# Performance work log

Measured on AMD Instinct MI355X. Metric: run time of the kernel, lower is better.

The kernel has to match this reference:

```python
import jax, jax.numpy as jnp
import numpy as np

B, S, D = 4, 8192, 512


def log_g(x):
    # torch: where(x>=0, log(relu(x)+0.5), -softplus(-x)); relu(x)+0.5 >= 0.5 so log is safe
    return jnp.where(x >= 0, jnp.log(jax.nn.relu(x) + 0.5), -jax.nn.softplus(-x))


def parallel_scan_log(log_coeffs, log_values):
    # log_coeffs: (B,S,D); log_values: (B,S+1,D)
    a_star = jnp.pad(jnp.cumsum(log_coeffs, axis=1), ((0, 0), (1, 0), (0, 0)))  # (B,S+1,D)
    log_h = a_star + jax.lax.cumlogsumexp(log_values - a_star, axis=1)
    return jnp.exp(log_h)[:, 1:]  # (B,S,D)


def setup_inputs() -> dict:
    key = jax.random.key(0)
    ks = jax.random.split(key, 7)
    scale = 1.0 / np.sqrt(D)
    x = jax.random.normal(ks[0], (B, S, D), dtype=jnp.float32)
    pre_h = jnp.zeros((B, 1, D), dtype=jnp.float32)
    Wf = jax.random.normal(ks[1], (D, D), dtype=jnp.float32) * scale
    bf = jax.random.normal(ks[2], (D,), dtype=jnp.float32) * 0.01
    Wi = jax.random.normal(ks[3], (D, D), dtype=jnp.float32) * scale
    bi = jax.random.normal(ks[4], (D,), dtype=jnp.float32) * 0.01
    Wh = jax.random.normal(ks[5], (D, D), dtype=jnp.float32) * scale
    bh = jax.random.normal(ks[6], (D,), dtype=jnp.float32) * 0.01
    return {"x": x, "pre_h": pre_h, "Wf": Wf, "bf": bf, "Wi": Wi, "bi": bi, "Wh": Wh, "bh": bh}


def reference(x, pre_h, Wf, bf, Wi, bi, Wh, bh):
    # gates: log(sigmoid(k)) = -softplus(-k)
    log_f = -jax.nn.softplus(-(jnp.einsum('bsd,de->bse', x, Wf) + bf))
    log_i = -jax.nn.softplus(-(jnp.einsum('bsd,de->bse', x, Wi) + bi))
    log_tilde_h = log_g(jnp.einsum('bsd,de->bse', x, Wh) + bh)
    log_pre_h = log_g(pre_h)  # (B,1,D)
    log_values = jnp.concatenate([log_pre_h, log_i + log_tilde_h], axis=1)  # (B,S+1,D)
    return parallel_scan_log(log_f, log_values)
```

## Files before the change

### kernel.cpp

```cpp
#include <hip/hip_runtime.h>
#include <hip/hip_bf16.h>

#define BATCH 4
#define SEQ   8192
#define DIM   512
#define M_TOT (BATCH*SEQ)
#define NCHUNK 128
#define CLEN   64

typedef __attribute__((ext_vector_type(4))) int int4v;

__device__ __forceinline__ float sigmoidf_(float x) {
    return 1.0f / (1.0f + __expf(-x));
}
__device__ __forceinline__ float gfun_(float x) {
    return (x >= 0.0f) ? (x + 0.5f) : sigmoidf_(x);
}

__device__ __forceinline__ void stage16(const void* g, void* lds) {
    __builtin_amdgcn_global_load_lds((const __attribute__((address_space(1))) void*)g,
                                     (__attribute__((address_space(3))) void*)lds,
                                     16, 0, 0);
}

__global__ __launch_bounds__(256) void quant_x(const float* __restrict__ x,
                                               char* __restrict__ xh, char* __restrict__ xl)
{
    const int t = blockIdx.x * 256 + threadIdx.x;
    float4 v = ((const float4*)x)[t];
    float vals[4] = {v.x, v.y, v.z, v.w};
    char hs[4], ls[4];
    #pragma unroll
    for (int e = 0; e < 4; ++e) {
        float c = fminf(fmaxf(vals[e], -15.8f), 15.8f);
        int q = (int)rintf(c * 2048.0f);
        int hi = (q + 128) >> 8;
        int lo = q - (hi << 8);
        hs[e] = (char)hi; ls[e] = (char)lo;
    }
    char4 hv = {hs[0], hs[1], hs[2], hs[3]};
    char4 lv = {ls[0], ls[1], ls[2], ls[3]};
    *(char4*)&xh[(size_t)t * 4] = hv;
    *(char4*)&xl[(size_t)t * 4] = lv;
}

__global__ __launch_bounds__(256) void quant_wT(
    const float* __restrict__ Wf, const float* __restrict__ Wi, const float* __restrict__ Wh,
    char* __restrict__ wth, char* __restrict__ wtl)
{
    __shared__ float tile[64][65];
    const int g = blockIdx.z;
    const float* W = (g == 0) ? Wf : (g == 1) ? Wi : Wh;
    const int k0 = blockIdx.x * 64, n0 = blockIdx.y * 64;
    const int c = threadIdx.x & 63, r4 = threadIdx.x >> 6;
    #pragma unroll
    for (int p = 0; p < 16; ++p) {
        int r = p * 4 + r4;
        tile[r][c] = W[(size_t)(k0 + r) * DIM + n0 + c];
    }
    __syncthreads();
    const size_t gbase = (size_t)g * DIM * DIM;
    #pragma unroll
    for (int p = 0; p < 16; ++p) {
        int nr = p * 4 + r4;
        float w = tile[c][nr];
        float cl = fminf(fmaxf(w, -0.49f), 0.49f);
        int q = (int)rintf(cl * 65536.0f);
        int hi = (q + 128) >> 8;
        int lo = q - (hi << 8);
        size_t o = gbase + (size_t)(n0 + nr) * DIM + k0 + c;
        wth[o] = (char)hi;
        wtl[o] = (char)lo;
    }
}

__device__ __forceinline__ void stage_tiles(
    const char* __restrict__ xhp, const char* __restrict__ xlp,
    const char* __restrict__ whp, const char* __restrict__ wlp,
    int m0, int n0, int k0,
    char (*A)[128][64], char (*B)[128][64], int wave, int lane)
{
    #pragma unroll
    for (int it = 0; it < 2; ++it) {
        const int grp = it * 4 + wave;
        const int mm  = grp * 16 + (lane >> 2);
        const int kb  = (lane & 3) * 16;
        const int ksw = kb ^ (((mm >> 1) & 3) << 4);
        stage16(xhp + (size_t)(m0 + mm) * DIM + k0 + ksw, &A[0][grp * 16][0]);
        stage16(xlp + (size_t)(m0 + mm) * DIM + k0 + ksw, &A[1][grp * 16][0]);
        stage16(whp + (size_t)(n0 + mm) * DIM + k0 + ksw, &B[0][grp * 16][0]);
        stage16(wlp + (size_t)(n0 + mm) * DIM + k0 + ksw, &B[1][grp * 16][0]);
    }
}

__global__ __launch_bounds__(256, 2) void gemm_i8(
    const char* __restrict__ xh, const char* __restrict__ xl,
    const char* __restrict__ wth, const char* __restrict__ wtl,
    const float* __restrict__ bfv, const float* __restrict__ biv, const float* __restrict__ bhv,
    float* __restrict__ fb, unsigned short* __restrict__ sib, unsigned short* __restrict__ ghb)
{
    __shared__ char sA[2][2][128][64];
    __shared__ char sB[2][2][128][64];

    const int bid = blockIdx.x;
    const int xr  = bid & 7;
    const int t   = bid >> 3;
    const int mmt = t / 12;
    const int gn  = t - mmt * 12;
    const int g   = gn >> 2;
    const int n0  = (gn & 3) * 128;
    const int m0  = (xr + (mmt << 3)) * 128;

    const int tid  = threadIdx.x;
    const int wave = tid >> 6;
    const int lane = tid & 63;
    const int wi = wave >> 1, wj = wave & 1;

    const char* wh_g = wth + (size_t)g * DIM * DIM;
    const char* wl_g = wtl + (size_t)g * DIM * DIM;

    int4v P2[4][4], P1[4][4];
    const int4v zero = {0, 0, 0, 0};
    #pragma unroll
    for (int i = 0; i < 4; ++i)
        #pragma unroll
        for (int j = 0; j < 4; ++j) { P2[i][j] = zero; P1[i][j] = zero; }

    stage_tiles(xh, xl, wh_g, wl_g, m0, n0, 0, sA[0], sB[0], wave, lane);
    __syncthreads();

    for (int kt = 0; kt < 8; ++kt) {
        const int cur = kt & 1;
        if (kt < 7) {
            stage_tiles(xh, xl, wh_g, wl_g, m0, n0, (kt + 1) * 64,
                        sA[cur ^ 1], sB[cur ^ 1], wave, lane);
        }
        const int kseg = (lane >> 4) * 16;
        int4v bhf[4], blf[4];
        #pragma unroll
        for (int j = 0; j < 4; ++j) {
            const int col = wj * 64 + j * 16 + (lane & 15);
            const int ks  = kseg ^ (((col >> 1) & 3) << 4);
            bhf[j] = *(const int4v*)&sB[cur][0][col][ks];
            blf[j] = *(const int4v*)&sB[cur][1][col][ks];
        }
        #pragma unroll
        for (int i = 0; i < 4; ++i) {
            const int row = wi * 64 + i * 16 + (lane & 15);
            const int ks  = kseg ^ (((row >> 1) & 3) << 4);
            int4v ahf = *(const int4v*)&sA[cur][0][row][ks];
            int4v alf = *(const int4v*)&sA[cur][1][row][ks];
            #pragma unroll
            for (int j = 0; j < 4; ++j) {
                P2[i][j] = __builtin_amdgcn_mfma_i32_16x16x64_i8(ahf, bhf[j], P2[i][j], 0, 0, 0);
                P1[i][j] = __builtin_amdgcn_mfma_i32_16x16x64_i8(ahf, blf[j], P1[i][j], 0, 0, 0);
                P1[i][j] = __builtin_amdgcn_mfma_i32_16x16x64_i8(alf, bhf[j], P1[i][j], 0, 0, 0);
            }
        }
        __syncthreads();
    }

    const float c2 = 1.0f / 2048.0f;
    const float c1 = 1.0f / 524288.0f;
    const float* bias = (g == 0) ? bfv : (g == 1) ? biv : bhv;
    #pragma unroll
    for (int j = 0; j < 4; ++j) {
        const int col = n0 + wj * 64 + j * 16 + (lane & 15);
        const float bv = bias[col];
        #pragma unroll
        for (int i = 0; i < 4; ++i) {
            #pragma unroll
            for (int r = 0; r < 4; ++r) {
                const float kv = (float)P2[i][j][r] * c2 + (float)P1[i][j][r] * c1 + bv;
                const int row = m0 + wi * 64 + i * 16 + (lane >> 4) * 4 + r;
                const size_t o = (size_t)row * DIM + col;
                if (g == 0) {
                    fb[o] = sigmoidf_(kv);
                } else if (g == 1) {
                    sib[o] = (unsigned short)fminf(rintf(sigmoidf_(kv) * 65536.0f), 65535.0f);
                } else {
                    ghb[o] = (unsigned short)fminf(rintf(gfun_(kv) * 8192.0f), 65535.0f);
                }
            }
        }
    }
}

#define VSCALE (1.0f / 536870912.0f)

__global__ __launch_bounds__(256) void scan_pass1(
    const float* __restrict__ fb,
    const unsigned short* __restrict__ sib, const unsigned short* __restrict__ ghb,
    float* __restrict__ Ach, float* __restrict__ Bch)
{
    const int d = blockIdx.x * 256 + threadIdx.x;
    const int c = blockIdx.y;
    const int b = blockIdx.z;
    float A = 1.0f, Bacc = 0.0f;
    size_t base = ((size_t)(b * SEQ + c * CLEN)) * DIM + d;
    #pragma unroll 4
    for (int t = 0; t < CLEN; ++t) {
        float f = fb[base + (size_t)t * DIM];
        float v = (float)sib[base + (size_t)t * DIM] *
                  (float)ghb[base + (size_t)t * DIM] * VSCALE;
        Bacc = fmaf(f, Bacc, v);
        A *= f;
    }
    const int idx = (b * NCHUNK + c) * DIM + d;
    Ach[idx] = A;
    Bch[idx] = Bacc;
}

__global__ __launch_bounds__(256) void scan_pass2(
    const float* __restrict__ pre_h,
    const float* __restrict__ Ach, const float* __restrict__ Bch,
    float* __restrict__ carry)
{
    const int gidx = blockIdx.x * 256 + threadIdx.x;
    const int b = gidx >> 9;
    const int d = gidx & (DIM - 1);
    float h = gfun_(pre_h[b * DIM + d]);
    for (int c = 0; c < NCHUNK; ++c) {
        const int idx = (b * NCHUNK + c) * DIM + d;
        carry[idx] = h;
        h = fmaf(Ach[idx], h, Bch[idx]);
    }
}

__global__ __launch_bounds__(256) void scan_pass3(
    const float* __restrict__ fb,
    const unsigned short* __restrict__ sib, const unsigned short* __restrict__ ghb,
    const float* __restrict__ carry, float* __restrict__ out)
{
    const int d = blockIdx.x * 256 + threadIdx.x;
    const int c = blockIdx.y;
    const int b = blockIdx.z;
    float h = carry[(b * NCHUNK + c) * DIM + d];
    size_t base = ((size_t)(b * SEQ + c * CLEN)) * DIM + d;
    #pragma unroll 4
    for (int t = 0; t < CLEN; ++t) {
        float f = fb[base + (size_t)t * DIM];
        float v = (float)sib[base + (size_t)t * DIM] *
                  (float)ghb[base + (size_t)t * DIM] * VSCALE;
        h = fmaf(f, h, v);
        out[base + (size_t)t * DIM] = h;
    }
}

extern "C" void kernel_launch(void* const* d_in, const int* in_sizes, int n_in,
                              void* d_out, int out_size, void* d_ws, size_t ws_size,
                              hipStream_t stream) {
    const float* x     = (const float*)d_in[0];
    const float* pre_h = (const float*)d_in[1];
    const float* Wf    = (const float*)d_in[2];
    const float* bf    = (const float*)d_in[3];
    const float* Wi    = (const float*)d_in[4];
    const float* bi    = (const float*)d_in[5];
    const float* Wh    = (const float*)d_in[6];
    const float* bh    = (const float*)d_in[7];
    float* out = (float*)d_out;

    char* ws = (char*)d_ws;
    const size_t XQ = (size_t)M_TOT * DIM;
    const size_t WQ = (size_t)3 * DIM * DIM;
    const size_t FB = (size_t)M_TOT * DIM * sizeof(float);
    const size_t UB = (size_t)M_TOT * DIM * 2;
    const size_t CH = (size_t)BATCH * NCHUNK * DIM * sizeof(float);

    char*  xh  = ws;
    char*  xl  = ws + XQ;
    char*  wth = ws + 2 * XQ;
    char*  wtl = ws + 2 * XQ + WQ;
    float* fbuf = (float*)(ws + 2 * XQ + 2 * WQ);
    unsigned short* sibuf = (unsigned short*)((char*)fbuf + FB);
    unsigned short* ghbuf = (unsigned short*)((char*)sibuf + UB);
    float* Ach   = (float*)((char*)ghbuf + UB);
    float* Bch   = (float*)((char*)Ach + CH);
    float* carry = (float*)((char*)Bch + CH);

    quant_x<<<(M_TOT * DIM / 4) / 256, 256, 0, stream>>>(x, xh, xl);
    quant_wT<<<dim3(8, 8, 3), 256, 0, stream>>>(Wf, Wi, Wh, wth, wtl);
    gemm_i8<<<3072, 256, 0, stream>>>(xh, xl, wth, wtl, bf, bi, bh, fbuf, sibuf, ghbuf);
    scan_pass1<<<dim3(DIM / 256, NCHUNK, BATCH), 256, 0, stream>>>(fbuf, sibuf, ghbuf, Ach, Bch);
    scan_pass2<<<(BATCH * DIM) / 256, 256, 0, stream>>>(pre_h, Ach, Bch, carry);
    scan_pass3<<<dim3(DIM / 256, NCHUNK, BATCH), 256, 0, stream>>>(fbuf, sibuf, ghbuf, carry, out);
}
```

Before: 311.1 us.

## Widen GEMM blocks, stage epilogue via LDS, vectorize scan kernels

The int8 GEMM now runs 512 threads per block, so each wave owns a 64x32 sub-tile, and each thread issues a single 16-byte async load per buffer. The 16-bit gate outputs are written through an LDS staging tile and stored as 16-byte rows to get coalesced writes. Scan passes 1 and 3 process four channels per thread with float4 and ushort4 loads, and pass 2 uses smaller blocks to spread across more CUs. The changes aim to cut memory transaction count and improve occupancy, but they raise register and LDS pressure per block.

```diff
diff --git a/kernel.cpp b/kernel.cpp
--- a/kernel.cpp
+++ b/kernel.cpp
@@ -9,6 +9,7 @@
 #define CLEN   64
 
 typedef __attribute__((ext_vector_type(4))) int int4v;
+typedef __attribute__((ext_vector_type(8))) unsigned short ushort8v;
 
 __device__ __forceinline__ float sigmoidf_(float x) {
     return 1.0f / (1.0f + __expf(-x));
@@ -74,33 +75,16 @@
     }
 }
 
-__device__ __forceinline__ void stage_tiles(
-    const char* __restrict__ xhp, const char* __restrict__ xlp,
-    const char* __restrict__ whp, const char* __restrict__ wlp,
-    int m0, int n0, int k0,
-    char (*A)[128][64], char (*B)[128][64], int wave, int lane)
-{
-    #pragma unroll
-    for (int it = 0; it < 2; ++it) {
-        const int grp = it * 4 + wave;
-        const int mm  = grp * 16 + (lane >> 2);
-        const int kb  = (lane & 3) * 16;
-        const int ksw = kb ^ (((mm >> 1) & 3) << 4);
-        stage16(xhp + (size_t)(m0 + mm) * DIM + k0 + ksw, &A[0][grp * 16][0]);
-        stage16(xlp + (size_t)(m0 + mm) * DIM + k0 + ksw, &A[1][grp * 16][0]);
-        stage16(whp + (size_t)(n0 + mm) * DIM + k0 + ksw, &B[0][grp * 16][0]);
-        stage16(wlp + (size_t)(n0 + mm) * DIM + k0 + ksw, &B[1][grp * 16][0]);
-    }
-}
-
-__global__ __launch_bounds__(256, 2) void gemm_i8(
+__global__ __launch_bounds__(512, 4) void gemm_i8(
     const char* __restrict__ xh, const char* __restrict__ xl,
     const char* __restrict__ wth, const char* __restrict__ wtl,
     const float* __restrict__ bfv, const float* __restrict__ biv, const float* __restrict__ bhv,
     float* __restrict__ fb, unsigned short* __restrict__ sib, unsigned short* __restrict__ ghb)
 {
-    __shared__ char sA[2][2][128][64];
-    __shared__ char sB[2][2][128][64];
+    __shared__ char smem[65536];
+    char (*sA)[2][128][64] = (char (*)[2][128][64])smem;
+    char (*sB)[2][128][64] = (char (*)[2][128][64])(smem + 32768);
+    unsigned short (*lds16)[136] = (unsigned short (*)[136])smem;
 
     const int bid = blockIdx.x;
     const int xr  = bid & 7;
@@ -114,32 +98,48 @@
     const int tid  = threadIdx.x;
     const int wave = tid >> 6;
     const int lane = tid & 63;
-    const int wi = wave >> 1, wj = wave & 1;
+    const int wi = wave >> 2, wj = wave & 3;
 
     const char* wh_g = wth + (size_t)g * DIM * DIM;
     const char* wl_g = wtl + (size_t)g * DIM * DIM;
 
-    int4v P2[4][4], P1[4][4];
+    const int smm  = tid >> 2;
+    const int skb  = (tid & 3) * 16;
+    const int sksw = skb ^ (((smm >> 1) & 3) << 4);
+    const int swrow = (tid >> 6) * 16;
+    const char* gx_h = xh   + (size_t)(m0 + smm) * DIM + sksw;
+    const char* gx_l = xl   + (size_t)(m0 + smm) * DIM + sksw;
+    const char* gw_h = wh_g + (size_t)(n0 + smm) * DIM + sksw;
+    const char* gw_l = wl_g + (size_t)(n0 + smm) * DIM + sksw;
+
+    int4v P2[4][2], P1[4][2];
     const int4v zero = {0, 0, 0, 0};
     #pragma unroll
     for (int i = 0; i < 4; ++i)
         #pragma unroll
-        for (int j = 0; j < 4; ++j) { P2[i][j] = zero; P1[i][j] = zero; }
-
-    stage_tiles(xh, xl, wh_g, wl_g, m0, n0, 0, sA[0], sB[0], wave, lane);
+        for (int j = 0; j < 2; ++j) { P2[i][j] = zero; P1[i][j] = zero; }
+
+    stage16(gx_h, &sA[0][0][swrow][0]);
+    stage16(gx_l, &sA[0][1][swrow][0]);
+    stage16(gw_h, &sB[0][0][swrow][0]);
+    stage16(gw_l, &sB[0][1][swrow][0]);
     __syncthreads();
 
     for (int kt = 0; kt < 8; ++kt) {
         const int cur = kt & 1;
         if (kt < 7) {
-            stage_tiles(xh, xl, wh_g, wl_g, m0, n0, (kt + 1) * 64,
-                        sA[cur ^ 1], sB[cur ^ 1], wave, lane);
+            const int nb = cur ^ 1;
+            const int ko = (kt + 1) * 64;
+            stage16(gx_h + ko, &sA[nb][0][swrow][0]);
+            stage16(gx_l + ko, &sA[nb][1][swrow][0]);
+            stage16(gw_h + ko, &sB[nb][0][swrow][0]);
+            stage16(gw_l + ko, &sB[nb][1][swrow][0]);
         }
         const int kseg = (lane >> 4) * 16;
-        int4v bhf[4], blf[4];
-        #pragma unroll
-        for (int j = 0; j < 4; ++j) {
-            const int col = wj * 64 + j * 16 + (lane & 15);
+        int4v bhf[2], blf[2];
+        #pragma unroll
+        for (int j = 0; j < 2; ++j) {
+            const int col = wj * 32 + j * 16 + (lane & 15);
             const int ks  = kseg ^ (((col >> 1) & 3) << 4);
             bhf[j] = *(const int4v*)&sB[cur][0][col][ks];
             blf[j] = *(const int4v*)&sB[cur][1][col][ks];
@@ -151,7 +151,7 @@
             int4v ahf = *(const int4v*)&sA[cur][0][row][ks];
             int4v alf = *(const int4v*)&sA[cur][1][row][ks];
             #pragma unroll
-            for (int j = 0; j < 4; ++j) {
+            for (int j = 0; j < 2; ++j) {
                 P2[i][j] = __builtin_amdgcn_mfma_i32_16x16x64_i8(ahf, bhf[j], P2[i][j], 0, 0, 0);
                 P1[i][j] = __builtin_amdgcn_mfma_i32_16x16x64_i8(ahf, blf[j], P1[i][j], 0, 0, 0);
                 P1[i][j] = __builtin_amdgcn_mfma_i32_16x16x64_i8(alf, bhf[j], P1[i][j], 0, 0, 0);
@@ -163,25 +163,49 @@
     const float c2 = 1.0f / 2048.0f;
     const float c1 = 1.0f / 524288.0f;
     const float* bias = (g == 0) ? bfv : (g == 1) ? biv : bhv;
-    #pragma unroll
-    for (int j = 0; j < 4; ++j) {
-        const int col = n0 + wj * 64 + j * 16 + (lane & 15);
-        const float bv = bias[col];
-        #pragma unroll
-        for (int i = 0; i < 4; ++i) {
+
+    if (g == 0) {
+        #pragma unroll
+        for (int j = 0; j < 2; ++j) {
+            const int col = n0 + wj * 32 + j * 16 + (lane & 15);
+            const float bv = bias[col];
             #pragma unroll
-            for (int r = 0; r < 4; ++r) {
-                const float kv = (float)P2[i][j][r] * c2 + (float)P1[i][j][r] * c1 + bv;
-                const int row = m0 + wi * 64 + i * 16 + (lane >> 4) * 4 + r;
-                const size_t o = (size_t)row * DIM + col;
-                if (g == 0) {
-                    fb[o] = sigmoidf_(kv);
-                } else if (g == 1) {
-                    sib[o] = (unsigned short)fminf(rintf(sigmoidf_(kv) * 65536.0f), 65535.0f);
-                } else {
-                    ghb[o] = (unsigned short)fminf(rintf(gfun_(kv) * 8192.0f), 65535.0f);
+            for (int i = 0; i < 4; ++i) {
+                #pragma unroll
+                for (int r = 0; r < 4; ++r) {
+                    const float kv = (float)P2[i][j][r] * c2 + (float)P1[i][j][r] * c1 + bv;
+                    const int row = m0 + wi * 64 + i * 16 + (lane >> 4) * 4 + r;
+                    fb[(size_t)row * DIM + col] = sigmoidf_(kv);
                 }
             }
+        }
+    } else {
+        #pragma unroll
+        for (int j = 0; j < 2; ++j) {
+            const int lc = wj * 32 + j * 16 + (lane & 15);
+            const float bv = bias[n0 + lc];
+            #pragma unroll
+            for (int i = 0; i < 4; ++i) {
+                #pragma unroll
+                for (int r = 0; r < 4; ++r) {
+                    const float kv = (float)P2[i][j][r] * c2 + (float)P1[i][j][r] * c1 + bv;
+                    const int lr = wi * 64 + i * 16 + (lane >> 4) * 4 + r;
+                    unsigned short q;
+                    if (g == 1) q = (unsigned short)fminf(rintf(sigmoidf_(kv) * 65536.0f), 65535.0f);
+                    else        q = (unsigned short)fminf(rintf(gfun_(kv) * 8192.0f), 65535.0f);
+                    lds16[lr][lc] = q;
+                }
+            }
+        }
+        __syncthreads();
+        unsigned short* outp = (g == 1) ? sib : ghb;
+        const int r  = tid >> 2;
+        const int cq = tid & 3;
+        #pragma unroll
+        for (int it = 0; it < 4; ++it) {
+            const int ci = cq + it * 4;
+            ushort8v vv = *(const ushort8v*)&lds16[r][ci * 8];
+            *(ushort8v*)&outp[(size_t)(m0 + r) * DIM + n0 + ci * 8] = vv;
         }
     }
 }
@@ -193,33 +217,42 @@
     const unsigned short* __restrict__ sib, const unsigned short* __restrict__ ghb,
     float* __restrict__ Ach, float* __restrict__ Bch)
 {
-    const int d = blockIdx.x * 256 + threadIdx.x;
-    const int c = blockIdx.y;
-    const int b = blockIdx.z;
-    float A = 1.0f, Bacc = 0.0f;
+    const int dq  = threadIdx.x & 127;
+    const int sub = threadIdx.x >> 7;
+    const int c = blockIdx.x * 2 + sub;
+    const int b = blockIdx.y;
+    const int d = dq * 4;
+    float A[4] = {1.f, 1.f, 1.f, 1.f};
+    float B[4] = {0.f, 0.f, 0.f, 0.f};
     size_t base = ((size_t)(b * SEQ + c * CLEN)) * DIM + d;
     #pragma unroll 4
     for (int t = 0; t < CLEN; ++t) {
-        float f = fb[base + (size_t)t * DIM];
-        float v = (float)sib[base + (size_t)t * DIM] *
-                  (float)ghb[base + (size_t)t * DIM] * VSCALE;
-        Bacc = fmaf(f, Bacc, v);
-        A *= f;
-    }
-    const int idx = (b * NCHUNK + c) * DIM + d;
-    Ach[idx] = A;
-    Bch[idx] = Bacc;
-}
-
-__global__ __launch_bounds__(256) void scan_pass2(
+        float4  f4 = *(const float4*)&fb[base + (size_t)t * DIM];
+        ushort4 s4 = *(const ushort4*)&sib[base + (size_t)t * DIM];
+        ushort4 g4 = *(const ushort4*)&ghb[base + (size_t)t * DIM];
+        float f[4] = {f4.x, f4.y, f4.z, f4.w};
+        float v[4] = {(float)s4.x * (float)g4.x * VSCALE,
+                      (float)s4.y * (float)g4.y * VSCALE,
+                      (float)s4.z * (float)g4.z * VSCALE,
+                      (float)s4.w * (float)g4.w * VSCALE};
+        #pragma unroll
+        for (int e = 0; e < 4; ++e) { B[e] = fmaf(f[e], B[e], v[e]); A[e] *= f[e]; }
+    }
+    const size_t idx = (size_t)(b * NCHUNK + c) * DIM + d;
+    *(float4*)&Ach[idx] = *(float4*)A;
+    *(float4*)&Bch[idx] = *(float4*)B;
+}
+
+__global__ __launch_bounds__(64) void scan_pass2(
     const float* __restrict__ pre_h,
     const float* __restrict__ Ach, const float* __restrict__ Bch,
     float* __restrict__ carry)
 {
-    const int gidx = blockIdx.x * 256 + threadIdx.x;
+    const int gidx = blockIdx.x * 64 + threadIdx.x;
     const int b = gidx >> 9;
     const int d = gidx & (DIM - 1);
     float h = gfun_(pre_h[b * DIM + d]);
+    #pragma unroll 4
     for (int c = 0; c < NCHUNK; ++c) {
         const int idx = (b * NCHUNK + c) * DIM + d;
         carry[idx] = h;
@@ -232,18 +265,28 @@
     const unsigned short* __restrict__ sib, const unsigned short* __restrict__ ghb,
     const float* __restrict__ carry, float* __restrict__ out)
 {
-    const int d = blockIdx.x * 256 + threadIdx.x;
-    const int c = blockIdx.y;
-    const int b = blockIdx.z;
-    float h = carry[(b * NCHUNK + c) * DIM + d];
+    const int dq  = threadIdx.x & 127;
+    const int sub = threadIdx.x >> 7;
+    const int c = blockIdx.x * 2 + sub;
+    const int b = blockIdx.y;
+    const int d = dq * 4;
+    float4 h4 = *(const float4*)&carry[(size_t)(b * NCHUNK + c) * DIM + d];
+    float h[4] = {h4.x, h4.y, h4.z, h4.w};
     size_t base = ((size_t)(b * SEQ + c * CLEN)) * DIM + d;
     #pragma unroll 4
     for (int t = 0; t < CLEN; ++t) {
-        float f = fb[base + (size_t)t * DIM];
-        float v = (float)sib[base + (size_t)t * DIM] *
-                  (float)ghb[base + (size_t)t * DIM] * VSCALE;
-        h = fmaf(f, h, v);
-        out[base + (size_t)t * DIM] = h;
+        float4  f4 = *(const float4*)&fb[base + (size_t)t * DIM];
+        ushort4 s4 = *(const ushort4*)&sib[base + (size_t)t * DIM];
+        ushort4 g4 = *(const ushort4*)&ghb[base + (size_t)t * DIM];
+        float f[4] = {f4.x, f4.y, f4.z, f4.w};
+        float v[4] = {(float)s4.x * (float)g4.x * VSCALE,
+                      (float)s4.y * (float)g4.y * VSCALE,
+                      (float)s4.z * (float)g4.z * VSCALE,
+                      (float)s4.w * (float)g4.w * VSCALE};
+        float o[4];
+        #pragma unroll
+        for (int e = 0; e < 4; ++e) { h[e] = fmaf(f[e], h[e], v[e]); o[e] = h[e]; }
+        *(float4*)&out[base + (size_t)t * DIM] = *(float4*)o;
     }
 }
 
@@ -280,8 +323,8 @@
 
     quant_x<<<(M_TOT * DIM / 4) / 256, 256, 0, stream>>>(x, xh, xl);
     quant_wT<<<dim3(8, 8, 3), 256, 0, stream>>>(Wf, Wi, Wh, wth, wtl);
-    gemm_i8<<<3072, 256, 0, stream>>>(xh, xl, wth, wtl, bf, bi, bh, fbuf, sibuf, ghbuf);
-    scan_pass1<<<dim3(DIM / 256, NCHUNK, BATCH), 256, 0, stream>>>(fbuf, sibuf, ghbuf, Ach, Bch);
-    scan_pass2<<<(BATCH * DIM) / 256, 256, 0, stream>>>(pre_h, Ach, Bch, carry);
-    scan_pass3<<<dim3(DIM / 256, NCHUNK, BATCH), 256, 0, stream>>>(fbuf, sibuf, ghbuf, carry, out);
-}
+    gemm_i8<<<3072, 512, 0, stream>>>(xh, xl, wth, wtl, bf, bi, bh, fbuf, sibuf, ghbuf);
+    scan_pass1<<<dim3(NCHUNK / 2, BATCH), 256, 0, stream>>>(fbuf, sibuf, ghbuf, Ach, Bch);
+    scan_pass2<<<32, 64, 0, stream>>>(pre_h, Ach, Bch, carry);
+    scan_pass3<<<dim3(NCHUNK / 2, BATCH), 256, 0, stream>>>(fbuf, sibuf, ghbuf, carry, out);
+}
```

Result: faster. 293.6 us (-5.6%).
